# Performance work log

Measured on AMD Instinct MI355X. Metric: run time of the kernel, lower is better.

## Reference

```python
import jax, jax.numpy as jnp
import numpy as np
from jax import lax

BINS = 256
HSIG = 0.01
MS_WEIGHTS = np.array([0.0448, 0.2856, 0.3001, 0.2363, 0.1333], dtype=np.float32)


def _conv(x, w, b=None, pad='SAME', groups=1):
    out = lax.conv_general_dilated(x, w, (1, 1), pad,
                                   feature_group_count=groups,
                                   dimension_numbers=('NCHW', 'OIHW', 'NCHW'))
    if b is not None:
        out = out + b[None, :, None, None]
    return out


def _avg_pool(x, k):
    B, C, H, W = x.shape
    return x.reshape(B, C, H // k, k, W // k, k).mean(axis=(3, 5))


def _max_pool2(x):
    return lax.reduce_window(x, -jnp.inf, lax.max, (1, 1, 2, 2), (1, 1, 2, 2), 'VALID')


def _gauss_win():
    c = jnp.arange(11, dtype=jnp.float32) - 5.0
    g = jnp.exp(-(c * c) / (2.0 * 1.5 * 1.5))
    return g / g.sum()


def _gauss_filter(x, win):
    C = x.shape[1]
    wh = jnp.tile(win.reshape(1, 1, 11, 1), (C, 1, 1, 1))
    ww = jnp.tile(win.reshape(1, 1, 1, 11), (C, 1, 1, 1))
    x = _conv(x, wh, pad='VALID', groups=C)
    return _conv(x, ww, pad='VALID', groups=C)


def _ssim(X, Y, win):
    C1, C2 = 0.01 ** 2, 0.03 ** 2
    mu1 = _gauss_filter(X, win)
    mu2 = _gauss_filter(Y, win)
    s11 = _gauss_filter(X * X, win) - mu1 * mu1
    s22 = _gauss_filter(Y * Y, win) - mu2 * mu2
    s12 = _gauss_filter(X * Y, win) - mu1 * mu2
    cs = (2.0 * s12 + C2) / (s11 + s22 + C2)
    ssim = ((2.0 * mu1 * mu2 + C1) / (mu1 * mu1 + mu2 * mu2 + C1)) * cs
    return ssim.mean(axis=(2, 3)), cs.mean(axis=(2, 3))  # (B,C) each


def _ms_ssim(X, Y):
    win = _gauss_win()
    vals = []
    for i in range(5):
        s, c = _ssim(X, Y, win)
        vals.append(jax.nn.relu(s if i == 4 else c))
        if i < 4:
            X = _avg_pool(X, 2)
            Y = _avg_pool(Y, 2)
    v = jnp.stack(vals)  # (5,B,C)
    w = jnp.asarray(MS_WEIGHTS)[:, None, None]
    return jnp.prod(v ** w, axis=0).mean()


def _soft_hist(y, edges):
    # faithful to source: broadcast every pixel against 256 Gaussian bins,
    # sum over dim 0 (batch), then normalize to a distribution.
    h = jnp.exp(-0.5 * ((y[..., None] - edges) / HSIG) ** 2).sum(axis=0)  # (C,H,W,BINS)
    return h / h.sum()


def _vgg_feats(x, ws, bs):
    # VGG19 features[:16]: conv1_1..conv3_3, maxpool after conv idx 1 and 3.
    for i, (w, b) in enumerate(zip(ws, bs)):
        x = jax.nn.relu(_conv(x, w, b))
        if i in (1, 3):
            x = _max_pool2(x)
    return x


def combined_loss(y_true, y_pred, ws, bs):
    B, C, H, W = y_pred.shape
    diff = y_pred - y_true
    ad = jnp.abs(diff)
    # smooth L1 (beta=1)
    l1 = jnp.mean(jnp.where(ad < 1.0, 0.5 * diff * diff, ad - 0.5))
    # MS-SSIM loss
    msssim_l = 1.0 - _ms_ssim(y_true, y_pred)
    # VGG perceptual
    f1 = _vgg_feats(y_true, ws, bs)
    f2 = _vgg_feats(y_pred, ws, bs)
    perc = jnp.mean((f1 - f2) ** 2)
    # soft histogram
    edges = jnp.linspace(0.0, 1.0, BINS, dtype=jnp.float32)
    hist_l = jnp.mean(jnp.abs(_soft_hist(y_true, edges) - _soft_hist(y_pred, edges)))
    # PSNR loss: 40 - (-10*log10(mse))
    mse = jnp.mean(diff * diff)
    psnr_l = 40.0 + 10.0 * jnp.log10(mse)
    # color loss
    color_l = jnp.mean(jnp.abs(y_true.mean(axis=(1, 2, 3)) - y_pred.mean(axis=(1, 2, 3))))
    # exposure loss (16x16 avg pool of channel mean, target 0.6)
    exp_l = jnp.mean((_avg_pool(y_pred.mean(axis=1, keepdims=True), 16) - 0.6) ** 2)
    # illumination smoothness (counts faithful to source)
    hv = jnp.sum((y_pred[:, :, 1:, :] - y_pred[:, :, :-1, :]) ** 2)
    wv = jnp.sum((y_pred[:, :, :, 1:] - y_pred[:, :, :, :-1]) ** 2)
    ill = 2.0 * (hv / ((W - 1) * C) + wv / (W * (C - 1))) / B
    # spatial consistency: 4 neighbor-difference kernels on 4x4-pooled luminance
    K = jnp.array([[[0, 0, 0], [-1, 1, 0], [0, 0, 0]],
                   [[0, 0, 0], [0, 1, -1], [0, 0, 0]],
                   [[0, -1, 0], [0, 1, 0], [0, 0, 0]],
                   [[0, 0, 0], [0, 1, 0], [0, -1, 0]]], dtype=jnp.float32)[:, None]  # (4,1,3,3)
    op = _avg_pool(y_true.mean(axis=1, keepdims=True), 4)
    ep = _avg_pool(y_pred.mean(axis=1, keepdims=True), 4)
    spat = jnp.sum((_conv(op, K) - _conv(ep, K)) ** 2, axis=1, keepdims=True)  # (B,1,H/4,W/4)
    total = (1.0 * l1 + 0.06 * perc + 0.05 * hist_l + 0.0083 * psnr_l
             + 0.25 * color_l + 0.5 * msssim_l + 0.1 * exp_l + 0.1 * ill + 0.1 * spat)
    return jnp.mean(total)


def setup_inputs() -> dict:
    key = jax.random.key(0)
    ks = jax.random.split(key, 16)
    B, H, W = 2, 224, 224
    y_true = jax.random.uniform(ks[0], (B, 3, H, W), dtype=jnp.float32)
    y_pred = jax.random.uniform(ks[1], (B, 3, H, W), dtype=jnp.float32)
    chans = [(64, 3), (64, 64), (128, 64), (128, 128), (256, 128), (256, 256), (256, 256)]
    inp = {'y_true': y_true, 'y_pred': y_pred}
    for i, (co, ci) in enumerate(chans):
        std = float(np.sqrt(2.0 / (ci * 9)))
        inp[f'w{i}'] = jax.random.normal(ks[2 + i], (co, ci, 3, 3), dtype=jnp.float32) * std
        inp[f'b{i}'] = jnp.zeros((co,), dtype=jnp.float32)
    return inp


def reference(y_true, y_pred, w0, w1, w2, w3, w4, w5, w6, b0, b1, b2, b3, b4, b5, b6):
    ws = [w0, w1, w2, w3, w4, w5, w6]
    bs = [b0, b1, b2, b3, b4, b5, b6]
    return combined_loss(y_true, y_pred, ws, bs)
```

## Files before the change

### kernel.cpp

```cpp
#include <hip/hip_runtime.h>
#include <cmath>

typedef __attribute__((ext_vector_type(8))) short  short8;
typedef __attribute__((ext_vector_type(4))) float  floatx4;
typedef __attribute__((ext_vector_type(8))) unsigned short ushort8;
typedef __attribute__((ext_vector_type(8))) unsigned char uchar8v;

#define SLOT(i) ((i) * 16)
#define ACC_L1   0
#define ACC_MSE  1
#define ACC_ST0  2
#define ACC_ST1  3
#define ACC_SP0  4
#define ACC_SP1  5
#define ACC_HV   6
#define ACC_WV   7
#define ACC_EXP  8
#define ACC_SPAT 9
#define ACC_PERC 10
#define SSIM_SLOT(scale, cs, img) (256 + ((scale) * 12 + (cs) * 6 + (img)) * 16)
#define ZPAGE_FLOAT_OFF 3200

struct GW { float g[11]; };

__device__ __forceinline__ float waveSum(float v) {
#pragma unroll
  for (int o = 32; o > 0; o >>= 1) v += __shfl_down(v, o, 64);
  return v;
}

__device__ __forceinline__ float blockSum256(float v) {
  __shared__ float red[4];
  const int tid = threadIdx.x;
  v = waveSum(v);
  __syncthreads();
  if ((tid & 63) == 0) red[tid >> 6] = v;
  __syncthreads();
  return red[0] + red[1] + red[2] + red[3];
}

__device__ __forceinline__ unsigned int pk_fp8x4(float v0, float v1, float v2, float v3) {
  int p = __builtin_amdgcn_cvt_pk_fp8_f32(v0, v1, 0, false);
  p = __builtin_amdgcn_cvt_pk_fp8_f32(v2, v3, p, true);
  return (unsigned int)p;
}

__device__ __forceinline__ void gload16(const unsigned char* g, unsigned char* l) {
  __builtin_amdgcn_global_load_lds(
      (const __attribute__((address_space(1))) void*)g,
      (__attribute__((address_space(3))) void*)l, 16, 0, 0);
}


struct PrepArgs {
  const float* w[6];
  int co[6], ci[6];
  int wcum[7];
  unsigned char* zp[6];
  int zH[6];
  int zcum[7];
};

struct MegaArgs {
  PrepArgs pa;
  unsigned char* wdst;
  const float* w0;
  const float* b0;
  unsigned char* c1;
  float* pyrX;
  float* pyrY;
  float* acc;
  int nPrep, nBasic, nPyr, nPS, nW4;
};

__global__ __launch_bounds__(256) void mega_k(MegaArgs A,
                                              const float* __restrict__ yt,
                                              const float* __restrict__ yp) {
  __shared__ float smem[684];
  const int tid = threadIdx.x;
  int bid = blockIdx.x;

  if (bid < A.nPrep) {
    const int idx = bid * 256 + tid;
    const PrepArgs& a = A.pa;
    if (idx < A.nW4) {
      const int e0 = idx * 4;
      int L = 0;
      while (e0 >= a.wcum[L + 1]) ++L;
      const int r = e0 - a.wcum[L];
      const int Cin = a.ci[L];
      const int cin = r % Cin;
      const int t = r / Cin;
      const int tap = t % 9;
      const int cout = t / 9;
      const float* wsrc = a.w[L] + ((size_t)cout * Cin + cin) * 9 + tap;
      *(unsigned int*)(A.wdst + e0) =
          pk_fp8x4(wsrc[0] * 8.f, wsrc[9] * 8.f, wsrc[18] * 8.f, wsrc[27] * 8.f);
      return;
    }
    const int zi = idx - A.nW4;
    if (zi >= a.zcum[6]) return;
    int b = 0;
    while (zi >= a.zcum[b + 1]) ++b;
    const int H = a.zH[b];
    const int rowE = (H + 2) * 32;
    const int perC = (2 * rowE + 2 * H * 32) >> 4;
    const int k = zi - a.zcum[b];
    const int pl = k / perC;
    const int k0 = (k - pl * perC) << 4;
    size_t o;
    if (k0 < rowE) o = k0;
    else if (k0 < 2 * rowE) o = (size_t)(H + 1) * rowE + (k0 - rowE);
    else {
      const int kk = k0 - 2 * rowE;
      const int y = kk / 64 + 1;
      const int r = kk & 63;
      o = (size_t)y * rowE + ((r < 32) ? (size_t)r : ((size_t)(H + 1) * 32 + (r - 32)));
    }
    *(uint4*)(a.zp[b] + (size_t)pl * (H + 2) * rowE + o) = (uint4){0, 0, 0, 0};
    return;
  }
  bid -= A.nPrep;

  if (bid < A.nBasic) {
    float* acc = A.acc;
    const int i4 = bid * 256 + tid;
    const int idx = i4 * 4;
    const float4 t4 = *(const float4*)(yt + idx);
    const float4 p4 = *(const float4*)(yp + idx);
    float l1 = 0.f, mse = 0.f, st0 = 0.f, st1 = 0.f, sp0 = 0.f, sp1 = 0.f, hv = 0.f, wv = 0.f;
#define BTERM(tt, pp) { const float d = (pp) - (tt); const float ad = fabsf(d); \
                        l1 += (ad < 1.f) ? 0.5f * d * d : ad - 0.5f; mse += d * d; }
    BTERM(t4.x, p4.x) BTERM(t4.y, p4.y) BTERM(t4.z, p4.z) BTERM(t4.w, p4.w)
#undef BTERM
    const float ts = t4.x + t4.y + t4.z + t4.w;
    const float ps = p4.x + p4.y + p4.z + p4.w;
    if (i4 < 37632) { st0 = ts; sp0 = ps; } else { st1 = ts; sp1 = ps; }
    const int h = (idx / 224) % 224;
    if (h < 223) {
      const float4 pn = *(const float4*)(yp + idx + 224);
      float d;
      d = pn.x - p4.x; hv += d * d;
      d = pn.y - p4.y; hv += d * d;
      d = pn.z - p4.z; hv += d * d;
      d = pn.w - p4.w; hv += d * d;
    }
    {
      const int w = idx % 224;
      float d;
      d = p4.y - p4.x; wv += d * d;
      d = p4.z - p4.y; wv += d * d;
      d = p4.w - p4.z; wv += d * d;
      if (w < 220) { d = yp[idx + 4] - p4.w; wv += d * d; }
    }
    float s;
    s = blockSum256(l1);  if (tid == 0) atomicAdd(acc + SLOT(ACC_L1), s);
    s = blockSum256(mse); if (tid == 0) atomicAdd(acc + SLOT(ACC_MSE), s);
    s = blockSum256(st0); if (tid == 0) atomicAdd(acc + SLOT(ACC_ST0), s);
    s = blockSum256(st1); if (tid == 0) atomicAdd(acc + SLOT(ACC_ST1), s);
    s = blockSum256(sp0); if (tid == 0) atomicAdd(acc + SLOT(ACC_SP0), s);
    s = blockSum256(sp1); if (tid == 0) atomicAdd(acc + SLOT(ACC_SP1), s);
    s = blockSum256(hv);  if (tid == 0) atomicAdd(acc + SLOT(ACC_HV), s);
    s = blockSum256(wv);  if (tid == 0) atomicAdd(acc + SLOT(ACC_WV), s);
    return;
  }
  bid -= A.nBasic;

  if (bid < A.nPyr) {
    float (*sA)[17] = (float(*)[17])smem;
    float (*s1)[9]  = (float(*)[9])(smem + 272);
    float (*s2)[5]  = (float(*)[5])(smem + 344);
    float (*s3)[3]  = (float(*)[3])(smem + 364);
    const int tile = bid % 196;
    const int img = (bid / 196) % 6;
    const int zt = bid / (196 * 6);
    const int ty = tile / 14, tx = tile - ty * 14;
    const float* src = (zt ? yp : yt) + (size_t)img * 224 * 224;
    float* dst = zt ? A.pyrY : A.pyrX;
    const int r = tid >> 4, c = tid & 15;
    sA[r][c] = src[(size_t)(ty * 16 + r) * 224 + tx * 16 + c];
    __syncthreads();
    if (tid < 64) {
      const int r1 = tid >> 3, c1 = tid & 7;
      const float m = 0.25f * (sA[2 * r1][2 * c1] + sA[2 * r1][2 * c1 + 1] +
                               sA[2 * r1 + 1][2 * c1] + sA[2 * r1 + 1][2 * c1 + 1]);
      dst[(size_t)img * 12544 + (ty * 8 + r1) * 112 + tx * 8 + c1] = m;
      s1[r1][c1] = m;
    }
    __syncthreads();
    if (tid < 16) {
      const int r2 = tid >> 2, c2 = tid & 3;
      const float m = 0.25f * (s1[2 * r2][2 * c2] + s1[2 * r2][2 * c2 + 1] +
                               s1[2 * r2 + 1][2 * c2] + s1[2 * r2 + 1][2 * c2 + 1]);
      dst[75264 + (size_t)img * 3136 + (ty * 4 + r2) * 56 + tx * 4 + c2] = m;
      s2[r2][c2] = m;
    }
    __syncthreads();
    if (tid < 4) {
      const int r3 = tid >> 1, c3 = tid & 1;
      const float m = 0.25f * (s2[2 * r3][2 * c3] + s2[2 * r3][2 * c3 + 1] +
                               s2[2 * r3 + 1][2 * c3] + s2[2 * r3 + 1][2 * c3 + 1]);
      dst[94080 + (size_t)img * 784 + (ty * 2 + r3) * 28 + tx * 2 + c3] = m;
      s3[r3][c3] = m;
    }
    __syncthreads();
    if (tid == 0) {
      const float m = 0.25f * (s3[0][0] + s3[0][1] + s3[1][0] + s3[1][1]);
      dst[98784 + (size_t)img * 196 + ty * 14 + tx] = m;
    }
    return;
  }
  bid -= A.nPyr;

  if (bid < A.nPS) {
    float* acc = A.acc;
    float (*sOp)[19] = (float(*)[19])smem;
    float (*sEp)[19] = (float(*)[19])(smem + 342);
    const int b = bid >> 4;
    const int tq = bid & 15;
    const int ty0 = (tq >> 2) * 16, tx0 = (tq & 3) * 16;
    for (int e = tid; e < 18 * 18; e += 256) {
      const int r = e / 18, c = e - (e / 18) * 18;
      const int gy = ty0 - 1 + r, gx = tx0 - 1 + c;
      float vo = 0.f, ve = 0.f;
      if (gy >= 0 && gy < 56 && gx >= 0 && gx < 56) {
        float so = 0.f, se = 0.f;
        for (int ch = 0; ch < 3; ++ch)
#pragma unroll
          for (int dy = 0; dy < 4; ++dy) {
            const size_t off = (((size_t)b * 3 + ch) * 224 + (gy * 4 + dy)) * 224 + gx * 4;
            const float4 a = *(const float4*)(yt + off);
            const float4 ee = *(const float4*)(yp + off);
            so += a.x + a.y + a.z + a.w;
            se += ee.x + ee.y + ee.z + ee.w;
          }
        vo = so * (1.f / 48.f);
        ve = se * (1.f / 48.f);
      }
      sOp[r][c] = vo; sEp[r][c] = ve;
    }
    __syncthreads();
    float v = 0.f;
    {
      const int r = tid >> 4, c = tid & 15;
      const int gy = ty0 + r, gx = tx0 + c;
      if (gy < 56 && gx < 56) {
        const float oc = sOp[r + 1][c + 1], ec = sEp[r + 1][c + 1];
        const float ol = sOp[r + 1][c],     el = sEp[r + 1][c];
        const float orr = sOp[r + 1][c + 2], er = sEp[r + 1][c + 2];
        const float ou = sOp[r][c + 1],     eu = sEp[r][c + 1];
        const float od = sOp[r + 2][c + 1], ed = sEp[r + 2][c + 1];
        float d;
        d = (oc - ol) - (ec - el);   v += d * d;
        d = (oc - orr) - (ec - er);  v += d * d;
        d = (oc - ou) - (ec - eu);   v += d * d;
        d = (oc - od) - (ec - ed);   v += d * d;
      }
    }
    const float t = blockSum256(v);
    if (tid == 0) atomicAdd(acc + SLOT(ACC_SPAT), t);
    if (tid < 16) {
      const int ey = tid >> 2, ex = tid & 3;
      if (ty0 + 4 * ey < 56 && tx0 + 4 * ex < 56) {
        float ssum = 0.f;
#pragma unroll
        for (int dy = 0; dy < 4; ++dy)
#pragma unroll
          for (int dx = 0; dx < 4; ++dx)
            ssum += sEp[4 * ey + dy + 1][4 * ex + dx + 1];
        const float m = ssum * (1.f / 16.f) - 0.6f;
        atomicAdd(acc + SLOT(ACC_EXP), m * m);
      }
    }
    return;
  }
  bid -= A.nPS;

  {
    float (*sIn)[10][12] = (float(*)[10][12])smem;
    const int zf = bid / 784;
    const int rem = bid - zf * 784;
    const int by = rem / 28, bx = rem - by * 28;
    const int tx = tid & 7, ty = (tid >> 3) & 7, tz = tid >> 6;
    const int img = zf >> 1;
    const int zb = zf & 1;
    const float* in = ((img >> 1) ? yp : yt) + (size_t)(img & 1) * 3 * 224 * 224;
    const int x0 = bx << 3, y0 = by << 3;
    const int x = x0 + tx, y = y0 + ty;
    int wrow = (zb * 32 + tz * 8) * 27;
    wrow = __builtin_amdgcn_readfirstlane(wrow);

    for (int el = tid; el < 300; el += 256) {
      const int ci = el / 100;
      const int r2 = el - ci * 100;
      const int r = r2 / 10, cl = r2 - r * 10;
      const int gy = y0 - 1 + r, gx = x0 - 1 + cl;
      float v = 0.f;
      if (gy >= 0 && gy < 224 && gx >= 0 && gx < 224)
        v = in[((size_t)ci * 224 + gy) * 224 + gx];
      sIn[ci][r][cl] = v;
    }
    __syncthreads();

    float a[8];
#pragma unroll
    for (int j = 0; j < 8; ++j) a[j] = 0.f;
#pragma unroll
    for (int ci = 0; ci < 3; ++ci) {
      float xv[9];
#pragma unroll
      for (int ky = 0; ky < 3; ++ky)
#pragma unroll
        for (int kx = 0; kx < 3; ++kx)
          xv[ky * 3 + kx] = sIn[ci][ty + ky][tx + kx];
      const float* wp = A.w0 + wrow + ci * 9;
#pragma unroll
      for (int j = 0; j < 8; ++j)
#pragma unroll
        for (int k = 0; k < 9; ++k)
          a[j] = fmaf(xv[k], wp[27 * j + k], a[j]);
    }
    const int coB = zb * 32 + tz * 8;
    float r[8];
#pragma unroll
    for (int j = 0; j < 8; ++j) r[j] = fmaxf(a[j] + A.b0[coB + j], 0.f);
    const size_t o = (((size_t)(zb * 4 + img) * 226 + (y + 1)) * 226 + (x + 1)) * 32 + tz * 8;
    uint2 rv;
    rv.x = pk_fp8x4(r[0], r[1], r[2], r[3]);
    rv.y = pk_fp8x4(r[4], r[5], r[6], r[7]);
    *(uint2*)(A.c1 + o) = rv;
  }
}

__global__ __launch_bounds__(256) void ssim_all_k(const float* __restrict__ yt,
                                                  const float* __restrict__ yp,
                                                  const float* __restrict__ pyrX,
                                                  const float* __restrict__ pyrY,
                                                  float* __restrict__ acc, GW gw) {
  __shared__ float sX[26][27], sY[26][27];
  __shared__ float sV[5][16][27];
  const int bid = blockIdx.x;
  int s = 0;
  if (bid >= 196) s = 1;
  if (bid >= 245) s = 2;
  if (bid >= 254) s = 3;
  if (bid >= 258) s = 4;
  const int cumA[5]   = {0, 196, 245, 254, 258};
  const int tilesA[5] = {14, 7, 3, 2, 1};
  const int dimsA[5]  = {224, 112, 56, 28, 14};
  const int offsA[5]  = {0, 0, 75264, 94080, 98784};
  const int t = bid - cumA[s];
  const int tiles = tilesA[s];
  const int n = dimsA[s];
  const int m = n - 10;
  const int tid = threadIdx.x;
  const int img = blockIdx.y;
  const int ty0 = (t / tiles) * 16;
  const int tx0 = (t - (t / tiles) * tiles) * 16;
  const float* Xb = ((s == 0) ? yt : pyrX + offsA[s]) + (size_t)img * n * n;
  const float* Yb = ((s == 0) ? yp : pyrY + offsA[s]) + (size_t)img * n * n;

  for (int e = tid; e < 26 * 26; e += 256) {
    const int r = e / 26, c = e - (e / 26) * 26;
    const int gy = ty0 + r, gx = tx0 + c;
    float xv = 0.f, yv = 0.f;
    if (gy < n && gx < n) {
      xv = Xb[(size_t)gy * n + gx];
      yv = Yb[(size_t)gy * n + gx];
    }
    sX[r][c] = xv; sY[r][c] = yv;
  }
  __syncthreads();

  for (int e = tid; e < 16 * 26; e += 256) {
    const int r = e / 26, c = e - (e / 26) * 26;
    float sx = 0.f, sy = 0.f, sxx = 0.f, syy = 0.f, sxy = 0.f;
#pragma unroll
    for (int tt = 0; tt < 11; ++tt) {
      const float xv = sX[r + tt][c];
      const float yv = sY[r + tt][c];
      const float g = gw.g[tt];
      sx += g * xv; sy += g * yv;
      sxx += g * xv * xv; syy += g * yv * yv; sxy += g * xv * yv;
    }
    sV[0][r][c] = sx; sV[1][r][c] = sy;
    sV[2][r][c] = sxx; sV[3][r][c] = syy; sV[4][r][c] = sxy;
  }
  __syncthreads();

  float sv = 0.f, cv = 0.f;
  {
    const int r = tid >> 4, c = tid & 15;
    if (ty0 + r < m && tx0 + c < m) {
      float mu1 = 0.f, mu2 = 0.f, e11 = 0.f, e22 = 0.f, e12 = 0.f;
#pragma unroll
      for (int tt = 0; tt < 11; ++tt) {
        const float g = gw.g[tt];
        mu1 += g * sV[0][r][c + tt];
        mu2 += g * sV[1][r][c + tt];
        e11 += g * sV[2][r][c + tt];
        e22 += g * sV[3][r][c + tt];
        e12 += g * sV[4][r][c + tt];
      }
      const float C1 = 1e-4f, C2 = 9e-4f;
      const float s11 = e11 - mu1 * mu1;
      const float s22 = e22 - mu2 * mu2;
      const float s12 = e12 - mu1 * mu2;
      cv = (2.f * s12 + C2) / (s11 + s22 + C2);
      sv = ((2.f * mu1 * mu2 + C1) / (mu1 * mu1 + mu2 * mu2 + C1)) * cv;
    }
  }
  float tsum = blockSum256(sv);
  if (tid == 0) atomicAdd(acc + SSIM_SLOT(s, 0, img), tsum);
  tsum = blockSum256(cv);
  if (tid == 0) atomicAdd(acc + SSIM_SLOT(s, 1, img), tsum);
}

template<int CIN, bool DB>
__global__ __launch_bounds__(256, (DB ? 2 : 4)) void conv_mfma(
    const unsigned char* __restrict__ in, const unsigned char* __restrict__ wtp,
    const float* __restrict__ bias, unsigned char* __restrict__ out,
    const float* __restrict__ zpage, int W, int rowsPI) {
  constexpr int NSLAB = CIN / 32;
  constexpr int NBUF = DB ? 2 : 1;
  constexpr int ASTB = 304;
  constexpr int BSTB = 48;
  constexpr int NBRUN = 6 * 66;
  constexpr int NPX = 66;
  constexpr int ASLOT = 32 * 19;
  constexpr int BSLOT = NBRUN * 3;
  constexpr int NAI = 3;
  constexpr int NBI = 5;
  __shared__ __align__(16) unsigned char As[NBUF][32 * ASTB];
  __shared__ __align__(16) unsigned char Bs[NBUF][NBRUN * BSTB];

  const int tid = threadIdx.x;
  const int lane = tid & 63;
  const int wave = tid >> 6;
  const int quad = lane >> 4;
  const int lr = lane & 15;
  const int img = blockIdx.y / rowsPI;
  const int y0 = (blockIdx.y - img * rowsPI) * 4;
  const int x0 = blockIdx.x * 64;
  const int cob = blockIdx.z * 32;
  const int Wp = W + 2;
  const int H = rowsPI * 4;
  const size_t IPL = (size_t)(H + 2) * Wp * 32;
  const unsigned char* inI = in + (size_t)img * IPL;
  unsigned char* outI = out + ((size_t)blockIdx.z * 4 + img) * IPL;

  floatx4 acc[2][4];
#pragma unroll
  for (int m = 0; m < 2; ++m)
#pragma unroll
    for (int n = 0; n < 4; ++n) acc[m][n] = (floatx4){0.f, 0.f, 0.f, 0.f};

  const int abase = lr * ASTB + quad * 8;

  const unsigned char* aptr[NAI];
  bool aok[NAI];
#pragma unroll
  for (int i = 0; i < NAI; ++i) {
    const int sl = tid + i * 256;
    aok[i] = sl < ASLOT;
    const int cout = aok[i] ? (sl / 19) : 0;
    const int r = sl - cout * 19;
    const int rr = (r >= 18) ? 17 : r;
    const int tap = rr >> 1, part = rr & 1;
    aptr[i] = wtp + ((size_t)(cob + cout) * 9 + tap) * CIN + part * 16;
  }
  const unsigned char* bptr[NBI];
  unsigned int bstep[NBI];
  bool bok[NBI];
#pragma unroll
  for (int i = 0; i < NBI; ++i) {
    const int sl = tid + i * 256;
    bok[i] = sl < BSLOT;
    const int run = sl / 3;
    const int r = sl - run * 3;
    const int part = (r >= 2) ? 1 : r;
    const int row = run / NPX;
    const int px = run - row * NPX;
    const int gx = x0 + px;
    if (bok[i] && gx < Wp) {
      bptr[i] = inI + ((size_t)(y0 + row) * Wp + gx) * 32 + part * 16;
      bstep[i] = (unsigned int)(4 * IPL);
    } else {
      bptr[i] = (const unsigned char*)zpage;
      bstep[i] = 0;
    }
  }

  auto stage = [&](int buf) {
#pragma unroll
    for (int i = 0; i < NAI; ++i)
      if (aok[i]) {
        gload16(aptr[i], As[buf] + (tid + i * 256) * 16);
        aptr[i] += 32;
      }
#pragma unroll
    for (int i = 0; i < NBI; ++i)
      if (bok[i]) {
        gload16(bptr[i], Bs[buf] + (tid + i * 256) * 16);
        bptr[i] += bstep[i];
      }
  };

  auto mfma_slab = [&](int buf) {
#pragma unroll
    for (int dy = 0; dy < 3; ++dy)
#pragma unroll
      for (int dx = 0; dx < 3; ++dx) {
        const int tap = dy * 3 + dx;
        const long af0 = *(const long*)(As[buf] + abase + tap * 32);
        const long af1 = *(const long*)(As[buf] + abase + 16 * ASTB + tap * 32);
        long bfr[4];
#pragma unroll
        for (int n = 0; n < 4; ++n)
          bfr[n] = *(const long*)(Bs[buf] + ((wave + dy) * NPX + n * 16 + lr + dx) * BSTB + quad * 8);
#pragma unroll
        for (int n = 0; n < 4; ++n) {
          acc[0][n] = __builtin_amdgcn_mfma_f32_16x16x32_fp8_fp8(af0, bfr[n], acc[0][n], 0, 0, 0);
          acc[1][n] = __builtin_amdgcn_mfma_f32_16x16x32_fp8_fp8(af1, bfr[n], acc[1][n], 0, 0, 0);
        }
      }
  };

  if constexpr (!DB) {
    for (int s = 0; s < NSLAB; ++s) {
      __syncthreads();
      stage(0);
      __syncthreads();
      mfma_slab(0);
    }
  } else {
    stage(0);
    __syncthreads();
    for (int s = 0; s < NSLAB; ++s) {
      const int cur = s & 1;
      if (s + 1 < NSLAB) stage(cur ^ 1);
      mfma_slab(cur);
      __syncthreads();
    }
  }

#pragma unroll
  for (int m = 0; m < 2; ++m) {
    const int cb = cob + m * 16 + quad * 4;
#pragma unroll
    for (int n = 0; n < 4; ++n) {
      const int px = x0 + n * 16 + lr;
      if (px < W) {
        const float v0 = fmaxf(acc[m][n].x * 0.125f + bias[cb + 0], 0.f);
        const float v1 = fmaxf(acc[m][n].y * 0.125f + bias[cb + 1], 0.f);
        const float v2 = fmaxf(acc[m][n].z * 0.125f + bias[cb + 2], 0.f);
        const float v3 = fmaxf(acc[m][n].w * 0.125f + bias[cb + 3], 0.f);
        *(unsigned int*)(outI + ((size_t)(y0 + wave + 1) * Wp + px + 1) * 32 +
                         m * 16 + quad * 4) = pk_fp8x4(v0, v1, v2, v3);
      }
    }
  }
}

__global__ __launch_bounds__(256) void pool_nhwc(const unsigned char* __restrict__ in,
                                                 unsigned char* __restrict__ out,
                                                 int Ho, int Wo, int C) {
  const int per = Ho * Wo * (C / 8);
  const int idx = blockIdx.x * 256 + threadIdx.x;
  if (idx >= 4 * per) return;
  const int img = idx / per;
  const int k = idx - img * per;
  const int c8 = k % (C / 8);
  const int p = k / (C / 8);
  const int x = p % Wo, y = p / Wo;
  const int zb = c8 >> 2;
  const int cw = (c8 & 3) * 8;
  const int Wi = 2 * Wo + 2;
  const unsigned char* ib = in + ((size_t)(zb * 4 + img) * (2 * Ho + 2) * Wi +
                                  (size_t)(2 * y + 1) * Wi + (2 * x + 1)) * 32 + cw;
  const uchar8v a = *(const uchar8v*)(ib);
  const uchar8v b = *(const uchar8v*)(ib + 32);
  const uchar8v d = *(const uchar8v*)(ib + (size_t)Wi * 32);
  const uchar8v e = *(const uchar8v*)(ib + (size_t)Wi * 32 + 32);
  const uchar8v r = __builtin_elementwise_max(__builtin_elementwise_max(a, b),
                                              __builtin_elementwise_max(d, e));
  *(uchar8v*)(out + ((size_t)(zb * 4 + img) * (Ho + 2) * (Wo + 2) +
                     (size_t)(y + 1) * (Wo + 2) + (x + 1)) * 32 + cw) = r;
}

#define FP8D(av, bv, J) { const float dd = __builtin_amdgcn_cvt_f32_fp8((av), (J)) - \
                                           __builtin_amdgcn_cvt_f32_fp8((bv), (J)); \
                          v = fmaf(dd, dd, v); }
__global__ __launch_bounds__(256) void perc_k(const unsigned char* __restrict__ f,
                                              float* __restrict__ acc) {
  const int PER = 56 * 56 * 256 / 8;
  const size_t PL = (size_t)58 * 58 * 32;
  float v = 0.f;
  for (int ch = blockIdx.x * 256 + threadIdx.x; ch < 2 * PER; ch += 256 * 256) {
    const int q = ch / PER;
    const int r = ch - q * PER;
    const int e = r * 8;
    const int c = e & 255;
    const int p = e >> 8;
    const int x = p % 56, y = p / 56;
    const int zb = c >> 5;
    const int cw = c & 31;
    const size_t o = (size_t)(zb * 4 + q) * PL + ((size_t)(y + 1) * 58 + (x + 1)) * 32 + cw;
    const uint2 a = *(const uint2*)(f + o);
    const uint2 b = *(const uint2*)(f + o + 2 * PL);
    FP8D(a.x, b.x, 0) FP8D(a.x, b.x, 1) FP8D(a.x, b.x, 2) FP8D(a.x, b.x, 3)
    FP8D(a.y, b.y, 0) FP8D(a.y, b.y, 1) FP8D(a.y, b.y, 2) FP8D(a.y, b.y, 3)
  }
  const float t = blockSum256(v);
  if (threadIdx.x == 0) atomicAdd(acc + SLOT(ACC_PERC), t);
}

__global__ void final_k(const float* __restrict__ acc, float* __restrict__ out) {
  if (threadIdx.x != 0 || blockIdx.x != 0) return;
  const float NPIX = 2.f * 3.f * 224.f * 224.f;
  const float l1 = acc[SLOT(ACC_L1)] / NPIX;
  const float mse = acc[SLOT(ACC_MSE)] / NPIX;
  const float psnr = 40.f + 10.f * log10f(mse);
  const float cm = 1.f / (3.f * 224.f * 224.f);
  const float color = 0.5f * (fabsf(acc[SLOT(ACC_ST0)] - acc[SLOT(ACC_SP0)]) +
                              fabsf(acc[SLOT(ACC_ST1)] - acc[SLOT(ACC_SP1)])) * cm;
  const float ill = acc[SLOT(ACC_HV)] / 669.f + acc[SLOT(ACC_WV)] / 448.f;
  const float expl = acc[SLOT(ACC_EXP)] / 392.f;
  const float spat = acc[SLOT(ACC_SPAT)] / 6272.f;
  const float perc = acc[SLOT(ACC_PERC)] / 1605632.f;
  const float wms[5] = {0.0448f, 0.2856f, 0.3001f, 0.2363f, 0.1333f};
  const int ns[5] = {214, 102, 46, 18, 4};
  float msum = 0.f;
  for (int img = 0; img < 6; ++img) {
    float prod = 1.f;
    for (int s = 0; s < 5; ++s) {
      const float denom = (float)(ns[s] * ns[s]);
      float v = (s == 4) ? acc[SSIM_SLOT(s, 0, img)] / denom
                         : acc[SSIM_SLOT(s, 1, img)] / denom;
      v = fmaxf(v, 0.f);
      prod *= powf(v, wms[s]);
    }
    msum += prod;
  }
  const float msssim = msum / 6.f;
  out[0] = l1 + 0.06f * perc + 0.0083f * psnr + 0.25f * color +
           0.5f * (1.f - msssim) + 0.1f * expl + 0.1f * ill + 0.1f * spat;
}

extern "C" void kernel_launch(void* const* d_in, const int* in_sizes, int n_in,
                              void* d_out, int out_size, void* d_ws, size_t ws_size,
                              hipStream_t stream) {
  const float* yt = (const float*)d_in[0];
  const float* yp = (const float*)d_in[1];
  const float* W7[7]; const float* B7[7];
  for (int i = 0; i < 7; ++i) {
    W7[i] = (const float*)d_in[2 + 2 * i];
    B7[i] = (const float*)d_in[3 + 2 * i];
  }

  char* ws = (char*)d_ws;
  float* acc = (float*)ws;
  const float* zpage = acc + ZPAGE_FLOAT_OFF;
  size_t off = 16384;
  auto align256 = [&]() { off = (off + 255) & ~(size_t)255; };
  align256(); unsigned char* C1  = (unsigned char*)(ws + off); off += (size_t)4 * 226 * 226 * 64;
  align256(); unsigned char* T0  = (unsigned char*)(ws + off); off += (size_t)4 * 226 * 226 * 64;
  align256(); unsigned char* Pl1 = (unsigned char*)(ws + off); off += (size_t)4 * 114 * 114 * 64;
  align256(); unsigned char* C3  = (unsigned char*)(ws + off); off += (size_t)4 * 114 * 114 * 128;
  align256(); unsigned char* Pl2 = (unsigned char*)(ws + off); off += (size_t)4 * 58 * 58 * 128;
  align256(); unsigned char* C5  = (unsigned char*)(ws + off); off += (size_t)4 * 58 * 58 * 256;
  align256(); unsigned char* C6  = (unsigned char*)(ws + off); off += (size_t)4 * 58 * 58 * 256;
  align256(); unsigned char* F   = (unsigned char*)(ws + off); off += (size_t)4 * 58 * 58 * 256;
  align256(); unsigned char* WT  = (unsigned char*)(ws + off); off += (size_t)1732608;
  align256(); float* pyrX = (float*)(ws + off); off += (size_t)100000 * 4;
  align256(); float* pyrY = (float*)(ws + off); off += (size_t)100000 * 4;
  if (ws_size < off) return;

  GW gw;
  {
    double vv[11]; double s = 0.0;
    for (int i = 0; i < 11; ++i) { const double c = i - 5.0; vv[i] = exp(-(c * c) / 4.5); s += vv[i]; }
    for (int i = 0; i < 11; ++i) gw.g[i] = (float)(vv[i] / s);
  }

  hipMemsetAsync(acc, 0, 16384, stream);

  const int co[7] = {64, 64, 128, 128, 256, 256, 256};
  const int ci[7] = {3, 64, 64, 128, 128, 256, 256};
  MegaArgs ma;
  size_t wtOff[7];
  {
    int e = 0;
    for (int i = 1; i < 7; ++i) {
      ma.pa.w[i - 1] = W7[i]; ma.pa.co[i - 1] = co[i]; ma.pa.ci[i - 1] = ci[i];
      ma.pa.wcum[i - 1] = e; wtOff[i] = (size_t)e; e += co[i] * 9 * ci[i];
    }
    ma.pa.wcum[6] = e;
    ma.nW4 = e / 4;
    unsigned char* bufs[6] = {C1, Pl1, C3, Pl2, C5, C6};
    const int hh[6] = {224, 112, 112, 56, 56, 56};
    const int cc[6] = {64, 64, 128, 128, 256, 256};
    int z = 0;
    for (int i = 0; i < 6; ++i) {
      ma.pa.zp[i] = bufs[i]; ma.pa.zH[i] = hh[i];
      ma.pa.zcum[i] = z;
      const int perC = (2 * (hh[i] + 2) * 32 + 2 * hh[i] * 32) >> 4;
      z += (4 * cc[i] / 32) * perC;
    }
    ma.pa.zcum[6] = z;
    ma.nPrep = (ma.nW4 + z + 255) / 256;
  }
  ma.wdst = WT;
  ma.w0 = W7[0]; ma.b0 = B7[0];
  ma.c1 = C1;
  ma.pyrX = pyrX; ma.pyrY = pyrY;
  ma.acc = acc;
  ma.nBasic = 294;
  ma.nPyr = 196 * 6 * 2;
  ma.nPS = 32;
  const int nConv1 = 28 * 28 * 8;
  const int megaBlocks = ma.nPrep + ma.nBasic + ma.nPyr + ma.nPS + nConv1;

  mega_k<<<megaBlocks, 256, 0, stream>>>(ma, yt, yp);
  ssim_all_k<<<dim3(259, 6), 256, 0, stream>>>(yt, yp, pyrX, pyrY, acc, gw);

  conv_mfma<64, false> <<<dim3(4, 4 * 56, 2), 256, 0, stream>>>(C1,  WT + wtOff[1], B7[1], T0, zpage, 224, 56);
  pool_nhwc<<<(4 * 112 * 112 * 8 + 255) / 256, 256, 0, stream>>>(T0, Pl1, 112, 112, 64);
  conv_mfma<64, false> <<<dim3(2, 4 * 28, 4), 256, 0, stream>>>(Pl1, WT + wtOff[2], B7[2], C3, zpage, 112, 28);
  conv_mfma<128, false><<<dim3(2, 4 * 28, 4), 256, 0, stream>>>(C3,  WT + wtOff[3], B7[3], T0, zpage, 112, 28);
  pool_nhwc<<<(4 * 56 * 56 * 16 + 255) / 256, 256, 0, stream>>>(T0, Pl2, 56, 56, 128);
  conv_mfma<128, true> <<<dim3(1, 4 * 14, 8), 256, 0, stream>>>(Pl2, WT + wtOff[4], B7[4], C5, zpage, 56, 14);
  conv_mfma<256, true> <<<dim3(1, 4 * 14, 8), 256, 0, stream>>>(C5,  WT + wtOff[5], B7[5], C6, zpage, 56, 14);
  conv_mfma<256, true> <<<dim3(1, 4 * 14, 8), 256, 0, stream>>>(C6,  WT + wtOff[6], B7[6], F,  zpage, 56, 14);
  perc_k<<<256, 256, 0, stream>>>(F, acc);

  final_k<<<1, 64, 0, stream>>>(acc, (float*)d_out);
}
```

Baseline: 269.9 us.

## Fuse SSIM tiles into conv2 kernel as extra grid blocks

```diff
diff --git a/kernel.cpp b/kernel.cpp
--- a/kernel.cpp
+++ b/kernel.cpp
@@ -49,6 +49,86 @@
   __builtin_amdgcn_global_load_lds(
       (const __attribute__((address_space(1))) void*)g,
       (__attribute__((address_space(3))) void*)l, 16, 0, 0);
+}
+
+__device__ __forceinline__ void ssim_tile(
+    int bid, int img, const float* __restrict__ yt, const float* __restrict__ yp,
+    const float* __restrict__ pyrX, const float* __restrict__ pyrY,
+    float* __restrict__ acc, const GW& gw,
+    float (*sX)[27], float (*sY)[27], float (*sV)[16][27]) {
+  int s = 0;
+  if (bid >= 196) s = 1;
+  if (bid >= 245) s = 2;
+  if (bid >= 254) s = 3;
+  if (bid >= 258) s = 4;
+  const int cumA[5]   = {0, 196, 245, 254, 258};
+  const int tilesA[5] = {14, 7, 3, 2, 1};
+  const int dimsA[5]  = {224, 112, 56, 28, 14};
+  const int offsA[5]  = {0, 0, 75264, 94080, 98784};
+  const int t = bid - cumA[s];
+  const int tiles = tilesA[s];
+  const int n = dimsA[s];
+  const int m = n - 10;
+  const int tid = threadIdx.x;
+  const int ty0 = (t / tiles) * 16;
+  const int tx0 = (t - (t / tiles) * tiles) * 16;
+  const float* Xb = ((s == 0) ? yt : pyrX + offsA[s]) + (size_t)img * n * n;
+  const float* Yb = ((s == 0) ? yp : pyrY + offsA[s]) + (size_t)img * n * n;
+
+  for (int e = tid; e < 26 * 26; e += 256) {
+    const int r = e / 26, c = e - (e / 26) * 26;
+    const int gy = ty0 + r, gx = tx0 + c;
+    float xv = 0.f, yv = 0.f;
+    if (gy < n && gx < n) {
+      xv = Xb[(size_t)gy * n + gx];
+      yv = Yb[(size_t)gy * n + gx];
+    }
+    sX[r][c] = xv; sY[r][c] = yv;
+  }
+  __syncthreads();
+
+  for (int e = tid; e < 16 * 26; e += 256) {
+    const int r = e / 26, c = e - (e / 26) * 26;
+    float sx = 0.f, sy = 0.f, sxx = 0.f, syy = 0.f, sxy = 0.f;
+#pragma unroll
+    for (int tt = 0; tt < 11; ++tt) {
+      const float xv = sX[r + tt][c];
+      const float yv = sY[r + tt][c];
+      const float g = gw.g[tt];
+      sx += g * xv; sy += g * yv;
+      sxx += g * xv * xv; syy += g * yv * yv; sxy += g * xv * yv;
+    }
+    sV[0][r][c] = sx; sV[1][r][c] = sy;
+    sV[2][r][c] = sxx; sV[3][r][c] = syy; sV[4][r][c] = sxy;
+  }
+  __syncthreads();
+
+  float sv = 0.f, cv = 0.f;
+  {
+    const int r = tid >> 4, c = tid & 15;
+    if (ty0 + r < m && tx0 + c < m) {
+      float mu1 = 0.f, mu2 = 0.f, e11 = 0.f, e22 = 0.f, e12 = 0.f;
+#pragma unroll
+      for (int tt = 0; tt < 11; ++tt) {
+        const float g = gw.g[tt];
+        mu1 += g * sV[0][r][c + tt];
+        mu2 += g * sV[1][r][c + tt];
+        e11 += g * sV[2][r][c + tt];
+        e22 += g * sV[3][r][c + tt];
+        e12 += g * sV[4][r][c + tt];
+      }
+      const float C1 = 1e-4f, C2 = 9e-4f;
+      const float s11 = e11 - mu1 * mu1;
+      const float s22 = e22 - mu2 * mu2;
+      const float s12 = e12 - mu1 * mu2;
+      cv = (2.f * s12 + C2) / (s11 + s22 + C2);
+      sv = ((2.f * mu1 * mu2 + C1) / (mu1 * mu1 + mu2 * mu2 + C1)) * cv;
+    }
+  }
+  float tsum = blockSum256(sv);
+  if (tid == 0) atomicAdd(acc + SSIM_SLOT(s, 0, img), tsum);
+  tsum = blockSum256(cv);
+  if (tid == 0) atomicAdd(acc + SSIM_SLOT(s, 1, img), tsum);
 }
 
 
@@ -332,90 +412,6 @@
   }
 }
 
-__global__ __launch_bounds__(256) void ssim_all_k(const float* __restrict__ yt,
-                                                  const float* __restrict__ yp,
-                                                  const float* __restrict__ pyrX,
-                                                  const float* __restrict__ pyrY,
-                                                  float* __restrict__ acc, GW gw) {
-  __shared__ float sX[26][27], sY[26][27];
-  __shared__ float sV[5][16][27];
-  const int bid = blockIdx.x;
-  int s = 0;
-  if (bid >= 196) s = 1;
-  if (bid >= 245) s = 2;
-  if (bid >= 254) s = 3;
-  if (bid >= 258) s = 4;
-  const int cumA[5]   = {0, 196, 245, 254, 258};
-  const int tilesA[5] = {14, 7, 3, 2, 1};
-  const int dimsA[5]  = {224, 112, 56, 28, 14};
-  const int offsA[5]  = {0, 0, 75264, 94080, 98784};
-  const int t = bid - cumA[s];
-  const int tiles = tilesA[s];
-  const int n = dimsA[s];
-  const int m = n - 10;
-  const int tid = threadIdx.x;
-  const int img = blockIdx.y;
-  const int ty0 = (t / tiles) * 16;
-  const int tx0 = (t - (t / tiles) * tiles) * 16;
-  const float* Xb = ((s == 0) ? yt : pyrX + offsA[s]) + (size_t)img * n * n;
-  const float* Yb = ((s == 0) ? yp : pyrY + offsA[s]) + (size_t)img * n * n;
-
-  for (int e = tid; e < 26 * 26; e += 256) {
-    const int r = e / 26, c = e - (e / 26) * 26;
-    const int gy = ty0 + r, gx = tx0 + c;
-    float xv = 0.f, yv = 0.f;
-    if (gy < n && gx < n) {
-      xv = Xb[(size_t)gy * n + gx];
-      yv = Yb[(size_t)gy * n + gx];
-    }
-    sX[r][c] = xv; sY[r][c] = yv;
-  }
-  __syncthreads();
-
-  for (int e = tid; e < 16 * 26; e += 256) {
-    const int r = e / 26, c = e - (e / 26) * 26;
-    float sx = 0.f, sy = 0.f, sxx = 0.f, syy = 0.f, sxy = 0.f;
-#pragma unroll
-    for (int tt = 0; tt < 11; ++tt) {
-      const float xv = sX[r + tt][c];
-      const float yv = sY[r + tt][c];
-      const float g = gw.g[tt];
-      sx += g * xv; sy += g * yv;
-      sxx += g * xv * xv; syy += g * yv * yv; sxy += g * xv * yv;
-    }
-    sV[0][r][c] = sx; sV[1][r][c] = sy;
-    sV[2][r][c] = sxx; sV[3][r][c] = syy; sV[4][r][c] = sxy;
-  }
-  __syncthreads();
-
-  float sv = 0.f, cv = 0.f;
-  {
-    const int r = tid >> 4, c = tid & 15;
-    if (ty0 + r < m && tx0 + c < m) {
-      float mu1 = 0.f, mu2 = 0.f, e11 = 0.f, e22 = 0.f, e12 = 0.f;
-#pragma unroll
-      for (int tt = 0; tt < 11; ++tt) {
-        const float g = gw.g[tt];
-        mu1 += g * sV[0][r][c + tt];
-        mu2 += g * sV[1][r][c + tt];
-        e11 += g * sV[2][r][c + tt];
-        e22 += g * sV[3][r][c + tt];
-        e12 += g * sV[4][r][c + tt];
-      }
-      const float C1 = 1e-4f, C2 = 9e-4f;
-      const float s11 = e11 - mu1 * mu1;
-      const float s22 = e22 - mu2 * mu2;
-      const float s12 = e12 - mu1 * mu2;
-      cv = (2.f * s12 + C2) / (s11 + s22 + C2);
-      sv = ((2.f * mu1 * mu2 + C1) / (mu1 * mu1 + mu2 * mu2 + C1)) * cv;
-    }
-  }
-  float tsum = blockSum256(sv);
-  if (tid == 0) atomicAdd(acc + SSIM_SLOT(s, 0, img), tsum);
-  tsum = blockSum256(cv);
-  if (tid == 0) atomicAdd(acc + SSIM_SLOT(s, 1, img), tsum);
-}
-
 template<int CIN, bool DB>
 __global__ __launch_bounds__(256, (DB ? 2 : 4)) void conv_mfma(
     const unsigned char* __restrict__ in, const unsigned char* __restrict__ wtp,
@@ -542,6 +538,150 @@
       mfma_slab(cur);
       __syncthreads();
     }
+  }
+
+#pragma unroll
+  for (int m = 0; m < 2; ++m) {
+    const int cb = cob + m * 16 + quad * 4;
+#pragma unroll
+    for (int n = 0; n < 4; ++n) {
+      const int px = x0 + n * 16 + lr;
+      if (px < W) {
+        const float v0 = fmaxf(acc[m][n].x * 0.125f + bias[cb + 0], 0.f);
+        const float v1 = fmaxf(acc[m][n].y * 0.125f + bias[cb + 1], 0.f);
+        const float v2 = fmaxf(acc[m][n].z * 0.125f + bias[cb + 2], 0.f);
+        const float v3 = fmaxf(acc[m][n].w * 0.125f + bias[cb + 3], 0.f);
+        *(unsigned int*)(outI + ((size_t)(y0 + wave + 1) * Wp + px + 1) * 32 +
+                         m * 16 + quad * 4) = pk_fp8x4(v0, v1, v2, v3);
+      }
+    }
+  }
+}
+
+__global__ __launch_bounds__(256, 4) void conv2_ssim_k(
+    const unsigned char* __restrict__ in, const unsigned char* __restrict__ wtp,
+    const float* __restrict__ bias, unsigned char* __restrict__ out,
+    const float* __restrict__ zpage,
+    const float* __restrict__ yt, const float* __restrict__ yp,
+    const float* __restrict__ pyrX, const float* __restrict__ pyrY,
+    float* __restrict__ acc_g, GW gw) {
+  constexpr int CIN = 64;
+  constexpr int NSLAB = CIN / 32;
+  constexpr int ASTB = 304;
+  constexpr int BSTB = 48;
+  constexpr int NBRUN = 6 * 66;
+  constexpr int NPX = 66;
+  constexpr int ASLOT = 32 * 19;
+  constexpr int BSLOT = NBRUN * 3;
+  constexpr int NAI = 3;
+  constexpr int NBI = 5;
+  const int W = 224, rowsPI = 56;
+  __shared__ __align__(16) unsigned char As[32 * ASTB];
+  __shared__ __align__(16) unsigned char Bs[NBRUN * BSTB];
+
+  const int tid = threadIdx.x;
+
+  if (blockIdx.z >= 2) {
+    const int sid = (blockIdx.z - 2) * 896 + blockIdx.y * 4 + blockIdx.x;
+    if (sid >= 1554) return;
+    const int img = sid / 259;
+    const int bid = sid - img * 259;
+    float (*sX)[27] = (float(*)[27])As;
+    float (*sY)[27] = (float(*)[27])(As + 2816);
+    float (*sV)[16][27] = (float(*)[16][27])Bs;
+    ssim_tile(bid, img, yt, yp, pyrX, pyrY, acc_g, gw, sX, sY, sV);
+    return;
+  }
+
+  const int lane = tid & 63;
+  const int wave = tid >> 6;
+  const int quad = lane >> 4;
+  const int lr = lane & 15;
+  const int img = blockIdx.y / rowsPI;
+  const int y0 = (blockIdx.y - img * rowsPI) * 4;
+  const int x0 = blockIdx.x * 64;
+  const int cob = blockIdx.z * 32;
+  const int Wp = W + 2;
+  const int H = rowsPI * 4;
+  const size_t IPL = (size_t)(H + 2) * Wp * 32;
+  const unsigned char* inI = in + (size_t)img * IPL;
+  unsigned char* outI = out + ((size_t)blockIdx.z * 4 + img) * IPL;
+
+  floatx4 acc[2][4];
+#pragma unroll
+  for (int m = 0; m < 2; ++m)
+#pragma unroll
+    for (int n = 0; n < 4; ++n) acc[m][n] = (floatx4){0.f, 0.f, 0.f, 0.f};
+
+  const int abase = lr * ASTB + quad * 8;
+
+  const unsigned char* aptr[NAI];
+  bool aok[NAI];
+#pragma unroll
+  for (int i = 0; i < NAI; ++i) {
+    const int sl = tid + i * 256;
+    aok[i] = sl < ASLOT;
+    const int cout = aok[i] ? (sl / 19) : 0;
+    const int r = sl - cout * 19;
+    const int rr = (r >= 18) ? 17 : r;
+    const int tap = rr >> 1, part = rr & 1;
+    aptr[i] = wtp + ((size_t)(cob + cout) * 9 + tap) * CIN + part * 16;
+  }
+  const unsigned char* bptr[NBI];
+  unsigned int bstep[NBI];
+  bool bok[NBI];
+#pragma unroll
+  for (int i = 0; i < NBI; ++i) {
+    const int sl = tid + i * 256;
+    bok[i] = sl < BSLOT;
+    const int run = sl / 3;
+    const int r = sl - run * 3;
+    const int part = (r >= 2) ? 1 : r;
+    const int row = run / NPX;
+    const int px = run - row * NPX;
+    const int gx = x0 + px;
+    if (bok[i] && gx < Wp) {
+      bptr[i] = inI + ((size_t)(y0 + row) * Wp + gx) * 32 + part * 16;
+      bstep[i] = (unsigned int)(4 * IPL);
+    } else {
+      bptr[i] = (const unsigned char*)zpage;
+      bstep[i] = 0;
+    }
+  }
+
+  for (int s = 0; s < NSLAB; ++s) {
+    __syncthreads();
+#pragma unroll
+    for (int i = 0; i < NAI; ++i)
+      if (aok[i]) {
+        gload16(aptr[i], As + (tid + i * 256) * 16);
+        aptr[i] += 32;
+      }
+#pragma unroll
+    for (int i = 0; i < NBI; ++i)
+      if (bok[i]) {
+        gload16(bptr[i], Bs + (tid + i * 256) * 16);
+        bptr[i] += bstep[i];
+      }
+    __syncthreads();
+
+#pragma unroll
+    for (int dy = 0; dy < 3; ++dy)
+#pragma unroll
+      for (int dx = 0; dx < 3; ++dx) {
+        const int tap = dy * 3 + dx;
+        const long af0 = *(const long*)(As + abase + tap * 32);
+        const long af1 = *(const long*)(As + abase + 16 * ASTB + tap * 32);
+        long bfr[4];
+#pragma unroll
+        for (int n = 0; n < 4; ++n)
+          bfr[n] = *(const long*)(Bs + ((wave + dy) * NPX + n * 16 + lr + dx) * BSTB + quad * 8);
+#pragma unroll
+        for (int n = 0; n < 4; ++n) {
+          acc[0][n] = __builtin_amdgcn_mfma_f32_16x16x32_fp8_fp8(af0, bfr[n], acc[0][n], 0, 0, 0);
+          acc[1][n] = __builtin_amdgcn_mfma_f32_16x16x32_fp8_fp8(af1, bfr[n], acc[1][n], 0, 0, 0);
+        }
+      }
   }
 
 #pragma unroll
@@ -722,9 +862,9 @@
   const int megaBlocks = ma.nPrep + ma.nBasic + ma.nPyr + ma.nPS + nConv1;
 
   mega_k<<<megaBlocks, 256, 0, stream>>>(ma, yt, yp);
-  ssim_all_k<<<dim3(259, 6), 256, 0, stream>>>(yt, yp, pyrX, pyrY, acc, gw);
-
-  conv_mfma<64, false> <<<dim3(4, 4 * 56, 2), 256, 0, stream>>>(C1,  WT + wtOff[1], B7[1], T0, zpage, 224, 56);
+
+  conv2_ssim_k<<<dim3(4, 224, 4), 256, 0, stream>>>(
+      C1, WT + wtOff[1], B7[1], T0, zpage, yt, yp, pyrX, pyrY, acc, gw);
   pool_nhwc<<<(4 * 112 * 112 * 8 + 255) / 256, 256, 0, stream>>>(T0, Pl1, 112, 112, 64);
   conv_mfma<64, false> <<<dim3(2, 4 * 28, 4), 256, 0, stream>>>(Pl1, WT + wtOff[2], B7[2], C3, zpage, 112, 28);
   conv_mfma<128, false><<<dim3(2, 4 * 28, 4), 256, 0, stream>>>(C3,  WT + wtOff[3], B7[3], T0, zpage, 112, 28);
```

Result: no change. 265.7 us (-1.5%).
